# Kernel tuning notes

Hardware: AMD Instinct MI355X
Metric: run time of the kernel (lower is better)

Reference implementation:

```python
import jax, jax.numpy as jnp
import numpy as np

C = 192
DCT = 7
EPS = 1e-5
LOW_X = [0,0,1,1,0,2,2,1,2,0,3,4,0,1,3,0,1,2,3,4,5,0,1,2,3,4,5,6,1,2,3,4]
LOW_Y = [0,1,0,1,2,0,1,2,2,3,0,0,4,3,1,5,4,3,2,1,0,6,5,4,3,2,1,0,6,5,4,3]


def _dct_basis():
    # basis[i, tx, ty] = bf(tx, ux_i, DCT) * bf(ty, vy_i, DCT)
    t = jnp.arange(DCT, dtype=jnp.float32)
    fx = jnp.array(LOW_X, dtype=jnp.float32)  # mapper scale = dct_h//7 = 1
    fy = jnp.array(LOW_Y, dtype=jnp.float32)
    def bf(freq):
        r = jnp.cos(jnp.pi * freq[:, None] * (t[None, :] + 0.5) / DCT) / jnp.sqrt(jnp.float32(DCT))
        return jnp.where(freq[:, None] == 0, r, r * jnp.sqrt(jnp.float32(2.0)))
    bx, by = bf(fx), bf(fy)  # [32, 7] each
    return bx[:, :, None] * by[:, None, :]  # [32, 7, 7]


def reference(x, wg1, bn2_g, bn2_b, bn2_m, bn2_v, wg2, bg2, beta, w1d, b1d, bn1_g, bn1_b, bn1_m, bn1_v):
    n, c, h, w = x.shape
    # gate: 1x1 conv -> BN2d (eval) -> ReLU -> global avg pool -> 1x1 conv
    g = jnp.einsum('nchw,oc->nohw', x, wg1)
    g = (g - bn2_m[None, :, None, None]) * (bn2_g / jnp.sqrt(bn2_v + EPS))[None, :, None, None] + bn2_b[None, :, None, None]
    g = jax.nn.relu(g).mean(axis=(2, 3))          # [n, 32]
    xg = g @ wg2.T + bg2                           # [n, 32]
    xg = jax.nn.relu(jnp.tanh(xg)) + beta          # gate_ac + beta
    # data-dependent channel partition from batch element 0 (torch uses .item() -> detached)
    xg0 = jax.lax.stop_gradient(xg[0])
    s = xg0.sum()
    p_mid = jnp.round(xg0[:31] / s * c)            # param[1..31]
    param = jnp.concatenate([jnp.zeros(1, jnp.float32), p_mid,
                             (jnp.float32(c) - p_mid.sum())[None]])  # [33]
    # build DCT filter: slice param[i]:param[i+1] gets basis i, later i overwrites
    ch = jnp.arange(c, dtype=jnp.float32)
    basis = _dct_basis()                           # [32, 7, 7]
    filt = jnp.zeros((c, DCT, DCT), jnp.float32)
    for i in range(32):
        m = (ch >= param[i]) & (ch < param[i + 1])
        filt = jnp.where(m[:, None, None], basis[i], filt)
    xp = x.reshape(n, c, DCT, h // DCT, DCT, w // DCT).mean(axis=(3, 5))
    y = jnp.sum(xp * filt[None], axis=(2, 3))      # [n, c] weighted spatial pooling
    # Conv1d(c, c, k=3, pad=1) on length-1 sequence: only center tap w1d[:, :, 1]
    y = y @ w1d[:, :, 1].T + b1d
    y = (y - bn1_m) * (bn1_g / jnp.sqrt(bn1_v + EPS)) + bn1_b
    y = jax.nn.relu(y)
    return x * y[:, :, None, None] + x


def setup_inputs() -> dict:
    key = jax.random.key(0)
    ks = jax.random.split(key, 16)
    n, h, w = 64, 56, 56
    return {
        'x':     jax.random.normal(ks[0], (n, C, h, w), jnp.float32),
        'wg1':   jax.random.normal(ks[1], (32, C), jnp.float32) * (2.0 / C) ** 0.5,
        'bn2_g': jax.random.uniform(ks[2], (32,), jnp.float32, 0.8, 1.2),
        'bn2_b': jax.random.normal(ks[3], (32,), jnp.float32) * 0.1,
        'bn2_m': jax.random.normal(ks[4], (32,), jnp.float32) * 0.1,
        'bn2_v': jax.random.uniform(ks[5], (32,), jnp.float32, 0.5, 1.5),
        'wg2':   jax.random.normal(ks[6], (32, 32), jnp.float32) * (2.0 / 32) ** 0.5,
        'bg2':   jax.random.normal(ks[7], (32,), jnp.float32) * 0.1,
        'beta':  jax.random.uniform(ks[8], (1,), jnp.float32, 0.05, 0.25),
        'w1d':   jax.random.normal(ks[9], (C, C, 3), jnp.float32) * (2.0 / (3 * C)) ** 0.5,
        'b1d':   jax.random.normal(ks[10], (C,), jnp.float32) * 0.1,
        'bn1_g': jax.random.uniform(ks[11], (C,), jnp.float32, 0.8, 1.2),
        'bn1_b': jax.random.normal(ks[12], (C,), jnp.float32) * 0.1,
        'bn1_m': jax.random.normal(ks[13], (C,), jnp.float32) * 0.1,
        'bn1_v': jax.random.uniform(ks[14], (C,), jnp.float32, 0.5, 1.5),
    }
```

## Files before the change

### kernel.cpp

```cpp
#include <hip/hip_runtime.h>
#include <hip/hip_bf16.h>
#include <math.h>

#define CCH 192
#define EPS 1e-5f

typedef float vfloat4 __attribute__((ext_vector_type(4)));

__device__ __constant__ int d_LOWX[32] = {0,0,1,1,0,2,2,1,2,0,3,4,0,1,3,0,1,2,3,4,5,0,1,2,3,4,5,6,1,2,3,4};
__device__ __constant__ int d_LOWY[32] = {0,1,0,1,2,0,1,2,2,3,0,0,4,3,1,5,4,3,2,1,0,6,5,4,3,2,1,0,6,5,4,3};

__global__ __launch_bounds__(256) void fused_pre_kernel(
    const float* __restrict__ x, const float* __restrict__ w1d,
    const float* __restrict__ wg1,
    const float* __restrict__ bn2_g, const float* __restrict__ bn2_b,
    const float* __restrict__ bn2_m, const float* __restrict__ bn2_v,
    float* __restrict__ xp, float* __restrict__ wt, float* __restrict__ partial) {
  __shared__ float smem[4 * 49];
  const int b = blockIdx.x;
  const int t = threadIdx.x;
  if (b >= 200) {
    const int pb = b - 200;
    const int n = pb / 48, c0 = (pb % 48) * 4;
    const int wv = t >> 6, l = t & 63;
    const int c = c0 + wv;
    const bool act = l < 56;
    const int lidx = act ? l : 0;
    const vfloat4* xv = (const vfloat4*)(x + (size_t)(n * CCH + c) * 3136);
    vfloat4 va[7], vb[7];
#pragma unroll
    for (int g = 0; g < 7; ++g) {
      va[g] = xv[g * 112 + lidx];
      vb[g] = xv[g * 112 + 56 + lidx];
    }
    float acc[7];
#pragma unroll
    for (int g = 0; g < 7; ++g) {
      float s = (va[g].x + va[g].y + va[g].z + va[g].w) +
                (vb[g].x + vb[g].y + vb[g].z + vb[g].w);
      acc[g] = act ? s : 0.f;
    }
#pragma unroll
    for (int g = 0; g < 7; ++g) {
      float a = acc[g] + __shfl_xor(acc[g], 1);
      a += __shfl(a, l + 28);
      a += __shfl(a, l + 14);
      if (act && l < 14 && (l & 1) == 0)
        smem[wv * 49 + g * 7 + (l >> 1)] = a;
    }
    __syncthreads();
    if (t < 196) xp[((size_t)n * CCH + c0) * 49 + t] = smem[t] * (1.f / 64.f);
  } else if (b >= 56) {
    const int i = (b - 56) * 256 + t;
    const int cc = i / CCH, k = i - cc * CCH;
    wt[k * CCH + cc] = w1d[cc * (CCH * 3) + 3 * k + 1];
  } else {
    const int h = b;
    const int wv = t >> 6, w = t & 63;
    float acc[8];
#pragma unroll
    for (int o = 0; o < 8; ++o) acc[o] = 0.f;
    const float* xrow = x + h * 56;
    for (int cc0 = 0; cc0 < CCH; cc0 += 8) {
      float xq[8];
#pragma unroll
      for (int j = 0; j < 8; ++j)
        xq[j] = (w < 56) ? xrow[(size_t)(cc0 + j) * 3136 + w] : 0.f;
#pragma unroll
      for (int j = 0; j < 8; ++j)
#pragma unroll
        for (int o = 0; o < 8; ++o)
          acc[o] += xq[j] * wg1[(wv * 8 + o) * CCH + cc0 + j];
    }
#pragma unroll
    for (int o = 0; o < 8; ++o) {
      const int oo = wv * 8 + o;
      float sc = bn2_g[oo] * rsqrtf(bn2_v[oo] + EPS);
      float v = acc[o] * sc + (bn2_b[oo] - bn2_m[oo] * sc);
      v = (w < 56) ? fmaxf(v, 0.f) : 0.f;
#pragma unroll
      for (int s = 1; s < 64; s <<= 1) v += __shfl_xor(v, s);
      if (w == 0) partial[h * 32 + oo] = v;
    }
  }
}

__global__ __launch_bounds__(256) void scale_kernel(
    const float* __restrict__ partial, const float* __restrict__ wg2,
    const float* __restrict__ bg2, const float* __restrict__ beta,
    const float* __restrict__ xp, const float* __restrict__ wt,
    const float* __restrict__ b1d,
    const float* __restrict__ bn1_g, const float* __restrict__ bn1_b,
    const float* __restrict__ bn1_m, const float* __restrict__ bn1_v,
    float* __restrict__ scale) {
  __shared__ float gm[32];
  __shared__ float xg[32];
  __shared__ float param[33];
  __shared__ float Btab[7][7];
  __shared__ float filt[CCH][49];
  __shared__ float yl[CCH];
  const int n = blockIdx.x, t = threadIdx.x;
  if (t < 32) {
    float s = 0.f;
    for (int hh = 0; hh < 56; ++hh) s += partial[hh * 32 + t];
    gm[t] = s * (1.f / 3136.f);
  }
  if (t < 49) {
    int f = t / 7, tt = t % 7;
    float r = cosf(3.14159265358979323846f * (float)f * ((float)tt + 0.5f) / 7.f) * rsqrtf(7.f);
    Btab[f][tt] = (f == 0) ? r : r * sqrtf(2.f);
  }
  __syncthreads();
  if (t < 32) {
    float a = bg2[t];
    for (int k = 0; k < 32; ++k) a += gm[k] * wg2[t * 32 + k];
    xg[t] = fmaxf(tanhf(a), 0.f) + beta[0];
  }
  __syncthreads();
  if (t == 0) {
    float s = 0.f;
    for (int k = 0; k < 32; ++k) s += xg[k];
    float psum = 0.f;
    param[0] = 0.f;
    for (int i = 0; i < 31; ++i) {
      float p = rintf(xg[i] / s * (float)CCH);
      param[i + 1] = p;
      psum += p;
    }
    param[32] = (float)CCH - psum;
  }
  __syncthreads();
  if (t < CCH) {
    int bi = -1;
    float cf = (float)t;
    for (int i = 0; i < 32; ++i)
      if (cf >= param[i] && cf < param[i + 1]) bi = i;
    int fx = (bi >= 0) ? d_LOWX[bi] : 0;
    int fy = (bi >= 0) ? d_LOWY[bi] : 0;
    for (int cell = 0; cell < 49; ++cell) {
      int a = cell / 7, bb = cell % 7;
      filt[t][cell] = (bi >= 0) ? Btab[fx][a] * Btab[fy][bb] : 0.f;
    }
  }
  __syncthreads();
  if (t < CCH) {
    const float* xc = xp + ((size_t)n * CCH + t) * 49;
    float s = 0.f;
#pragma unroll
    for (int cell = 0; cell < 49; ++cell) s += xc[cell] * filt[t][cell];
    yl[t] = s;
  }
  __syncthreads();
  if (t < CCH) {
    float acc = b1d[t];
#pragma unroll 8
    for (int k = 0; k < CCH; ++k) acc += yl[k] * wt[k * CCH + t];
    float sc = bn1_g[t] * rsqrtf(bn1_v[t] + EPS);
    float v = (acc - bn1_m[t]) * sc + bn1_b[t];
    scale[n * CCH + t] = 1.f + fmaxf(v, 0.f);
  }
}

__global__ __launch_bounds__(256) void apply_kernel(
    const float* __restrict__ x, const float* __restrict__ scale,
    float* __restrict__ out) {
  const int base = blockIdx.x * 2048 + threadIdx.x;
  const vfloat4* __restrict__ xv = (const vfloat4*)x;
  vfloat4* __restrict__ ov = (vfloat4*)out;
#pragma unroll
  for (int k = 0; k < 8; ++k) {
    const int f = base + k * 256;
    const float s = scale[f / 784];
    vfloat4 v = xv[f];
    ov[f] = v * s;
  }
}

extern "C" void kernel_launch(void* const* d_in, const int* in_sizes, int n_in,
                              void* d_out, int out_size, void* d_ws, size_t ws_size,
                              hipStream_t stream) {
  const float* x     = (const float*)d_in[0];
  const float* wg1   = (const float*)d_in[1];
  const float* bn2_g = (const float*)d_in[2];
  const float* bn2_b = (const float*)d_in[3];
  const float* bn2_m = (const float*)d_in[4];
  const float* bn2_v = (const float*)d_in[5];
  const float* wg2   = (const float*)d_in[6];
  const float* bg2   = (const float*)d_in[7];
  const float* beta  = (const float*)d_in[8];
  const float* w1d   = (const float*)d_in[9];
  const float* b1d   = (const float*)d_in[10];
  const float* bn1_g = (const float*)d_in[11];
  const float* bn1_b = (const float*)d_in[12];
  const float* bn1_m = (const float*)d_in[13];
  const float* bn1_v = (const float*)d_in[14];
  float* out = (float*)d_out;

  float* ws      = (float*)d_ws;
  float* partial = ws;
  float* filt    = partial + 1792;
  float* wt      = filt + 9408;
  float* xp      = wt + 36864;
  float* scale   = xp + 602112;

  fused_pre_kernel<<<3272, 256, 0, stream>>>(x, w1d, wg1, bn2_g, bn2_b, bn2_m, bn2_v,
                                             xp, wt, partial);
  scale_kernel<<<64, 256, 0, stream>>>(partial, wg2, bg2, beta, xp, wt, b1d,
                                       bn1_g, bn1_b, bn1_m, bn1_v, scale);
  apply_kernel<<<4704, 256, 0, stream>>>(x, scale, out);
}
```

Before: 340.1 us.

## Fuse all three stages into one cooperative persistent kernel with grid syncs

Replaces the three-kernel sequence with a single cooperative kernel of 768 blocks. The blocks split the gate conv rows and the pooling tiles, then grid.sync, compute the per-batch scales in 64 blocks, grid.sync again, and apply the scale using nontemporal stores. The intent is to remove launch gaps and inter-kernel drain, and to keep x partly cache-resident between passes. The scale kernel also drops its shared filter table and computes weights inline. Risks are grid-sync cost, most blocks sitting idle during the scale phase, and reduced parallelism in the apply phase.

```diff
diff --git a/kernel.cpp b/kernel.cpp
--- a/kernel.cpp
+++ b/kernel.cpp
@@ -1,14 +1,180 @@
 #include <hip/hip_runtime.h>
-#include <hip/hip_bf16.h>
+#include <hip/hip_cooperative_groups.h>
 #include <math.h>
 
 #define CCH 192
 #define EPS 1e-5f
+#define NBLK 768
+#define POOLB 712
 
 typedef float vfloat4 __attribute__((ext_vector_type(4)));
+
+namespace cg = cooperative_groups;
 
 __device__ __constant__ int d_LOWX[32] = {0,0,1,1,0,2,2,1,2,0,3,4,0,1,3,0,1,2,3,4,5,0,1,2,3,4,5,6,1,2,3,4};
 __device__ __constant__ int d_LOWY[32] = {0,1,0,1,2,0,1,2,2,3,0,0,4,3,1,5,4,3,2,1,0,6,5,4,3,2,1,0,6,5,4,3};
+
+__global__ __launch_bounds__(256, 4) void fused_all(
+    const float* __restrict__ x, const float* __restrict__ wg1,
+    const float* __restrict__ bn2_g, const float* __restrict__ bn2_b,
+    const float* __restrict__ bn2_m, const float* __restrict__ bn2_v,
+    const float* __restrict__ wg2, const float* __restrict__ bg2,
+    const float* __restrict__ beta, const float* __restrict__ w1d,
+    const float* __restrict__ b1d,
+    const float* __restrict__ bn1_g, const float* __restrict__ bn1_b,
+    const float* __restrict__ bn1_m, const float* __restrict__ bn1_v,
+    float* __restrict__ out,
+    float* __restrict__ partial, float* __restrict__ wt,
+    float* __restrict__ xp, float* __restrict__ scale) {
+  cg::grid_group grid = cg::this_grid();
+  __shared__ float smem[4 * 49];
+  __shared__ float gm[32], xg[32], param[33], Btab[49], yl[CCH];
+  const int b = blockIdx.x, t = threadIdx.x;
+
+  if (b >= POOLB) {
+    const int h = b - POOLB;
+    const int wv = t >> 6, w = t & 63;
+    float acc[8];
+#pragma unroll
+    for (int o = 0; o < 8; ++o) acc[o] = 0.f;
+    const float* xrow = x + h * 56;
+    for (int cc0 = 0; cc0 < CCH; cc0 += 8) {
+      float xq[8];
+#pragma unroll
+      for (int j = 0; j < 8; ++j)
+        xq[j] = (w < 56) ? xrow[(size_t)(cc0 + j) * 3136 + w] : 0.f;
+#pragma unroll
+      for (int j = 0; j < 8; ++j)
+#pragma unroll
+        for (int o = 0; o < 8; ++o)
+          acc[o] += xq[j] * wg1[(wv * 8 + o) * CCH + cc0 + j];
+    }
+#pragma unroll
+    for (int o = 0; o < 8; ++o) {
+      const int oo = wv * 8 + o;
+      float sc = bn2_g[oo] * rsqrtf(bn2_v[oo] + EPS);
+      float v = acc[o] * sc + (bn2_b[oo] - bn2_m[oo] * sc);
+      v = (w < 56) ? fmaxf(v, 0.f) : 0.f;
+#pragma unroll
+      for (int s = 1; s < 64; s <<= 1) v += __shfl_xor(v, s);
+      if (w == 0) partial[h * 32 + oo] = v;
+    }
+  } else {
+    if (b < 144) {
+      const int i = b * 256 + t;
+      const int cc = i / CCH, k = i - cc * CCH;
+      wt[k * CCH + cc] = w1d[cc * (CCH * 3) + 3 * k + 1];
+    }
+    for (int u = b; u < 3072; u += POOLB) {
+      const int n = u / 48, c0 = (u % 48) * 4;
+      const int wv = t >> 6, l = t & 63;
+      const int c = c0 + wv;
+      const bool act = l < 56;
+      const int lidx = act ? l : 0;
+      const vfloat4* xv = (const vfloat4*)(x + (size_t)(n * CCH + c) * 3136);
+      vfloat4 va[7], vb[7];
+#pragma unroll
+      for (int g = 0; g < 7; ++g) {
+        va[g] = xv[g * 112 + lidx];
+        vb[g] = xv[g * 112 + 56 + lidx];
+      }
+      float as[7];
+#pragma unroll
+      for (int g = 0; g < 7; ++g) {
+        float s = (va[g].x + va[g].y + va[g].z + va[g].w) +
+                  (vb[g].x + vb[g].y + vb[g].z + vb[g].w);
+        as[g] = act ? s : 0.f;
+      }
+      __syncthreads();
+#pragma unroll
+      for (int g = 0; g < 7; ++g) {
+        float a = as[g] + __shfl_xor(as[g], 1);
+        a += __shfl(a, l + 28);
+        a += __shfl(a, l + 14);
+        if (act && l < 14 && (l & 1) == 0)
+          smem[wv * 49 + g * 7 + (l >> 1)] = a;
+      }
+      __syncthreads();
+      if (t < 196) xp[((size_t)n * CCH + c0) * 49 + t] = smem[t] * (1.f / 64.f);
+    }
+  }
+
+  grid.sync();
+
+  if (b < 64) {
+    const int n = b;
+    if (t < 32) {
+      float s = 0.f;
+      for (int hh = 0; hh < 56; ++hh) s += partial[hh * 32 + t];
+      gm[t] = s * (1.f / 3136.f);
+    }
+    if (t < 49) {
+      int f = t / 7, tt = t % 7;
+      float r = cosf(3.14159265358979323846f * (float)f * ((float)tt + 0.5f) / 7.f) * rsqrtf(7.f);
+      Btab[t] = (f == 0) ? r : r * sqrtf(2.f);
+    }
+    __syncthreads();
+    if (t < 32) {
+      float a = bg2[t];
+      for (int k = 0; k < 32; ++k) a += gm[k] * wg2[t * 32 + k];
+      xg[t] = fmaxf(tanhf(a), 0.f) + beta[0];
+    }
+    __syncthreads();
+    if (t == 0) {
+      float s = 0.f;
+      for (int k = 0; k < 32; ++k) s += xg[k];
+      float psum = 0.f;
+      param[0] = 0.f;
+      for (int i = 0; i < 31; ++i) {
+        float p = rintf(xg[i] / s * (float)CCH);
+        param[i + 1] = p;
+        psum += p;
+      }
+      param[32] = (float)CCH - psum;
+    }
+    __syncthreads();
+    if (t < CCH) {
+      int bi = -1;
+      float cf = (float)t;
+      for (int i = 0; i < 32; ++i)
+        if (cf >= param[i] && cf < param[i + 1]) bi = i;
+      int fx = (bi >= 0) ? d_LOWX[bi] : 0;
+      int fy = (bi >= 0) ? d_LOWY[bi] : 0;
+      const float* xc = xp + ((size_t)n * CCH + t) * 49;
+      float s = 0.f;
+      for (int cell = 0; cell < 49; ++cell) {
+        int a = cell / 7, bb = cell - a * 7;
+        float w = Btab[fx * 7 + a] * Btab[fy * 7 + bb];
+        s += xc[cell] * ((bi >= 0) ? w : 0.f);
+      }
+      yl[t] = s;
+    }
+    __syncthreads();
+    if (t < CCH) {
+      float acc = b1d[t];
+#pragma unroll 8
+      for (int k = 0; k < CCH; ++k) acc += yl[k] * wt[k * CCH + t];
+      float sc = bn1_g[t] * rsqrtf(bn1_v[t] + EPS);
+      float v = (acc - bn1_m[t]) * sc + bn1_b[t];
+      scale[n * CCH + t] = 1.f + fmaxf(v, 0.f);
+    }
+  }
+
+  grid.sync();
+
+  {
+    const int base = b * 12544 + t;
+    const vfloat4* __restrict__ xv = (const vfloat4*)x;
+    vfloat4* __restrict__ ov = (vfloat4*)out;
+#pragma unroll 7
+    for (int k = 0; k < 49; ++k) {
+      const int f = base + k * 256;
+      const float s = scale[f / 784];
+      vfloat4 v = xv[f];
+      __builtin_nontemporal_store(v * s, ov + f);
+    }
+  }
+}
 
 __global__ __launch_bounds__(256) void fused_pre_kernel(
     const float* __restrict__ x, const float* __restrict__ w1d,
@@ -33,16 +199,16 @@
       va[g] = xv[g * 112 + lidx];
       vb[g] = xv[g * 112 + 56 + lidx];
     }
-    float acc[7];
+    float as[7];
 #pragma unroll
     for (int g = 0; g < 7; ++g) {
       float s = (va[g].x + va[g].y + va[g].z + va[g].w) +
                 (vb[g].x + vb[g].y + vb[g].z + vb[g].w);
-      acc[g] = act ? s : 0.f;
+      as[g] = act ? s : 0.f;
     }
 #pragma unroll
     for (int g = 0; g < 7; ++g) {
-      float a = acc[g] + __shfl_xor(acc[g], 1);
+      float a = as[g] + __shfl_xor(as[g], 1);
       a += __shfl(a, l + 28);
       a += __shfl(a, l + 14);
       if (act && l < 14 && (l & 1) == 0)
@@ -96,8 +262,7 @@
   __shared__ float gm[32];
   __shared__ float xg[32];
   __shared__ float param[33];
-  __shared__ float Btab[7][7];
-  __shared__ float filt[CCH][49];
+  __shared__ float Btab[49];
   __shared__ float yl[CCH];
   const int n = blockIdx.x, t = threadIdx.x;
   if (t < 32) {
@@ -108,7 +273,7 @@
   if (t < 49) {
     int f = t / 7, tt = t % 7;
     float r = cosf(3.14159265358979323846f * (float)f * ((float)tt + 0.5f) / 7.f) * rsqrtf(7.f);
-    Btab[f][tt] = (f == 0) ? r : r * sqrtf(2.f);
+    Btab[t] = (f == 0) ? r : r * sqrtf(2.f);
   }
   __syncthreads();
   if (t < 32) {
@@ -137,17 +302,13 @@
       if (cf >= param[i] && cf < param[i + 1]) bi = i;
     int fx = (bi >= 0) ? d_LOWX[bi] : 0;
     int fy = (bi >= 0) ? d_LOWY[bi] : 0;
-    for (int cell = 0; cell < 49; ++cell) {
-      int a = cell / 7, bb = cell % 7;
-      filt[t][cell] = (bi >= 0) ? Btab[fx][a] * Btab[fy][bb] : 0.f;
-    }
-  }
-  __syncthreads();
-  if (t < CCH) {
     const float* xc = xp + ((size_t)n * CCH + t) * 49;
     float s = 0.f;
-#pragma unroll
-    for (int cell = 0; cell < 49; ++cell) s += xc[cell] * filt[t][cell];
+    for (int cell = 0; cell < 49; ++cell) {
+      int a = cell / 7, bb = cell - a * 7;
+      float w = Btab[fx * 7 + a] * Btab[fy * 7 + bb];
+      s += xc[cell] * ((bi >= 0) ? w : 0.f);
+    }
     yl[t] = s;
   }
   __syncthreads();
@@ -203,9 +364,29 @@
   float* xp      = wt + 36864;
   float* scale   = xp + 602112;
 
-  fused_pre_kernel<<<3272, 256, 0, stream>>>(x, w1d, wg1, bn2_g, bn2_b, bn2_m, bn2_v,
-                                             xp, wt, partial);
-  scale_kernel<<<64, 256, 0, stream>>>(partial, wg2, bg2, beta, xp, wt, b1d,
-                                       bn1_g, bn1_b, bn1_m, bn1_v, scale);
-  apply_kernel<<<4704, 256, 0, stream>>>(x, scale, out);
-}
+  static int coop = -1;
+  if (coop < 0) {
+    int dev = 0, v = 0;
+    hipGetDevice(&dev);
+    hipDeviceGetAttribute(&v, hipDeviceAttributeCooperativeLaunch, dev);
+    coop = v;
+  }
+
+  hipError_t e = hipErrorUnknown;
+  if (coop) {
+    void* args[] = {(void*)&x, (void*)&wg1, (void*)&bn2_g, (void*)&bn2_b,
+                    (void*)&bn2_m, (void*)&bn2_v, (void*)&wg2, (void*)&bg2,
+                    (void*)&beta, (void*)&w1d, (void*)&b1d, (void*)&bn1_g,
+                    (void*)&bn1_b, (void*)&bn1_m, (void*)&bn1_v, (void*)&out,
+                    (void*)&partial, (void*)&wt, (void*)&xp, (void*)&scale};
+    e = hipLaunchCooperativeKernel((const void*)fused_all, dim3(NBLK), dim3(256),
+                                   args, 0, stream);
+  }
+  if (e != hipSuccess) {
+    fused_pre_kernel<<<3272, 256, 0, stream>>>(x, w1d, wg1, bn2_g, bn2_b, bn2_m, bn2_v,
+                                               xp, wt, partial);
+    scale_kernel<<<64, 256, 0, stream>>>(partial, wg2, bg2, beta, xp, wt, b1d,
+                                         bn1_g, bn1_b, bn1_m, bn1_v, scale);
+    apply_kernel<<<4704, 256, 0, stream>>>(x, scale, out);
+  }
+}
```

Result: slower. 529.0 us (+55.6%).
